# Kernel optimization log

Hardware: AMD Instinct MI355X
Metric: run time of the kernel (lower is better)

Reference implementation:

```python
import jax, jax.numpy as jnp
import numpy as np

N, F_IN, H, D = 4096, 512, 4, 64  # nodes, in_features, num_heads, head_dim (out_features = H*D = 256)
NEG_BIG = -9e15


def setup_inputs() -> dict:
    key = jax.random.key(0)
    k_x, k_adj, k_W, k_a = jax.random.split(key, 4)
    x = jax.random.normal(k_x, (N, F_IN), dtype=jnp.float32)
    adj = jax.random.randint(k_adj, (N, N), 0, 2, dtype=jnp.int32)
    # xavier_uniform-like scales
    W = jax.random.normal(k_W, (H, F_IN, D), dtype=jnp.float32) * np.float32((6.0 / (F_IN + D)) ** 0.5)
    a = jax.random.normal(k_a, (H, 2 * D), dtype=jnp.float32) * np.float32(0.1)
    bias = jnp.zeros((H * D,), dtype=jnp.float32)
    return {"x": x, "adj": adj, "W": W, "a": a, "bias": bias}


def reference(x, adj, W, a, bias):
    # Wx per head: [H, N, D]
    Wx = jnp.einsum('nf,hfd->hnd', x, W)
    # e[h,i,j] = leaky_relu(a[h,:D].Wx[h,i] + a[h,D:].Wx[h,j]) -- same math as concat form
    s_src = jnp.einsum('hnd,hd->hn', Wx, a[:, :D])  # [H, N]
    s_dst = jnp.einsum('hnd,hd->hn', Wx, a[:, D:])  # [H, N]
    e = jax.nn.leaky_relu(s_src[:, :, None] + s_dst[:, None, :], negative_slope=0.2)  # [H, N, N]
    masked = jnp.where(adj[None, :, :] > 0, e, jnp.float32(NEG_BIG))
    att = jax.nn.softmax(masked, axis=-1)  # row-wise softmax, [H, N, N]
    h = jnp.einsum('hij,hjd->hid', att, Wx)  # [H, N, D]
    out = h.transpose(1, 0, 2).reshape(x.shape[0], -1) + bias  # [N, H*D]
    return jax.nn.relu(out)
```

## Files before the change

### kernel.cpp

```cpp
#include <hip/hip_runtime.h>
#include <hip/hip_bf16.h>

#define NN   4096
#define FIN  512
#define NH   4
#define DD   64

typedef float f32x4 __attribute__((ext_vector_type(4)));
typedef short s16x8 __attribute__((ext_vector_type(8)));

__device__ __forceinline__ short bfbits(float f) {
  union { float f; unsigned u; } v; v.f = f;
  unsigned r = v.u + 0x7FFFu + ((v.u >> 16) & 1u);
  return (short)(r >> 16);
}

__device__ __forceinline__ int pkbf(float a, float b) {
  union { float f; unsigned u; } va, vb;
  va.f = a; vb.f = b;
  unsigned ra = (va.u + 0x7FFFu + ((va.u >> 16) & 1u)) >> 16;
  unsigned rb = (vb.u + 0x7FFFu + ((vb.u >> 16) & 1u)) & 0xFFFF0000u;
  return (int)(ra | rb);
}

__device__ __forceinline__ float hexp2(float x) {
#if __has_builtin(__builtin_amdgcn_exp2f)
  return __builtin_amdgcn_exp2f(x);
#else
  return __builtin_exp2f(x);
#endif
}

__global__ __launch_bounds__(512, 4) void gat_pre(
    const int* __restrict__ adj, const float* __restrict__ x,
    const float* __restrict__ W, const float* __restrict__ a,
    unsigned long long* __restrict__ bits, short* __restrict__ V2,
    float* __restrict__ ssrc, float* __restrict__ sdst)
{
  __shared__ __align__(16) char sm[34816];
  short* As = (short*)sm;
  short* Bs = (short*)(sm + 17408);
  float* Cs = (float*)sm;

  const int b = blockIdx.x;
  const int t = threadIdx.x;
  const int w = t >> 6, lane = t & 63;

  const int g3 = b / 3, m3 = b - g3 * 3;
  if (m3 < 2) {
    const int row = g3 * 2 + m3 + ((w) << 9);
    const int pb = g3 * 2 + m3;
    const int rrow = (pb << 3) | w;
    const int* arow = adj + (size_t)rrow * NN;
    unsigned long long mine = 0;
#pragma unroll 8
    for (int it = 0; it < 64; ++it) {
      int v = arow[it * 64 + lane];
      unsigned long long bl = __ballot(v != 0);
      if (lane == it) mine = bl;
    }
    bits[(size_t)rrow * 64 + lane] = mine;
    (void)row;
    return;
  }

  const int b2 = g3;
  const int h  = b2 >> 6;
  const int r  = b2 & 63;
  const int n0 = r * 64;
  const int lm = lane & 15, q = lane >> 4;
  const int rs = w & 3, cs = w >> 2;

  f32x4 acc[2] = {};
  const float* Wh = W + (size_t)h * (FIN * DD);

  for (int kq = 0; kq < 4; ++kq) {
    {
      const int row = t >> 3, fl = (t & 7) * 16;
      const float* xp = x + (size_t)(n0 + row) * FIN + kq * 128 + fl;
      float4 v0 = ((const float4*)xp)[0];
      float4 v1 = ((const float4*)xp)[1];
      float4 v2 = ((const float4*)xp)[2];
      float4 v3 = ((const float4*)xp)[3];
      union { short s[8]; int4 v; } u0, u1;
      u0.s[0]=bfbits(v0.x); u0.s[1]=bfbits(v0.y); u0.s[2]=bfbits(v0.z); u0.s[3]=bfbits(v0.w);
      u0.s[4]=bfbits(v1.x); u0.s[5]=bfbits(v1.y); u0.s[6]=bfbits(v1.z); u0.s[7]=bfbits(v1.w);
      u1.s[0]=bfbits(v2.x); u1.s[1]=bfbits(v2.y); u1.s[2]=bfbits(v2.z); u1.s[3]=bfbits(v2.w);
      u1.s[4]=bfbits(v3.x); u1.s[5]=bfbits(v3.y); u1.s[6]=bfbits(v3.z); u1.s[7]=bfbits(v3.w);
      *(int4*)(As + row * 136 + fl)     = u0.v;
      *(int4*)(As + row * 136 + fl + 8) = u1.v;
    }
    {
      const int fl = t >> 2, dc = (t & 3) * 16;
      const float* wp = Wh + (size_t)(kq * 128 + fl) * DD + dc;
      float4 w0 = ((const float4*)wp)[0];
      float4 w1 = ((const float4*)wp)[1];
      float4 w2 = ((const float4*)wp)[2];
      float4 w3 = ((const float4*)wp)[3];
      Bs[(dc+ 0)*136+fl]=bfbits(w0.x); Bs[(dc+ 1)*136+fl]=bfbits(w0.y);
      Bs[(dc+ 2)*136+fl]=bfbits(w0.z); Bs[(dc+ 3)*136+fl]=bfbits(w0.w);
      Bs[(dc+ 4)*136+fl]=bfbits(w1.x); Bs[(dc+ 5)*136+fl]=bfbits(w1.y);
      Bs[(dc+ 6)*136+fl]=bfbits(w1.z); Bs[(dc+ 7)*136+fl]=bfbits(w1.w);
      Bs[(dc+ 8)*136+fl]=bfbits(w2.x); Bs[(dc+ 9)*136+fl]=bfbits(w2.y);
      Bs[(dc+10)*136+fl]=bfbits(w2.z); Bs[(dc+11)*136+fl]=bfbits(w2.w);
      Bs[(dc+12)*136+fl]=bfbits(w3.x); Bs[(dc+13)*136+fl]=bfbits(w3.y);
      Bs[(dc+14)*136+fl]=bfbits(w3.z); Bs[(dc+15)*136+fl]=bfbits(w3.w);
    }
    __syncthreads();
#pragma unroll
    for (int s = 0; s < 4; ++s) {
      s16x8 af = *(const s16x8*)(As + (rs * 16 + lm) * 136 + s * 32 + q * 8);
#pragma unroll
      for (int c = 0; c < 2; ++c) {
        s16x8 bf = *(const s16x8*)(Bs + (cs * 32 + c * 16 + lm) * 136 + s * 32 + q * 8);
        acc[c] = __builtin_amdgcn_mfma_f32_16x16x32_bf16(af, bf, acc[c], 0, 0, 0);
      }
    }
    __syncthreads();
  }

#pragma unroll
  for (int c = 0; c < 2; ++c)
#pragma unroll
    for (int g = 0; g < 4; ++g)
      Cs[(cs * 32 + c * 16 + lm) * 65 + (rs * 16 + q * 4 + g)] = acc[c][g];
  __syncthreads();

  {
    const int d = t >> 3, nc = (t & 7) * 8;
    union { short s[8]; int4 v; } u;
#pragma unroll
    for (int e = 0; e < 8; ++e) u.s[e] = bfbits(Cs[d * 65 + nc + e]);
    *(int4*)(V2 + ((size_t)(h * 128 + r * 2 + (nc >> 5)) * 64 + d) * 32 + (nc & 31)) = u.v;
  }
  if (t < 128) {
    const int n = t & 63;
    const int isdst = t >> 6;
    const float* av = a + h * 128 + isdst * 64;
    float s = 0.f;
#pragma unroll 8
    for (int d = 0; d < 64; ++d) s = fmaf(Cs[d * 65 + n], av[d], s);
    const float LOG2E = 1.4426950408889634f;
    (isdst ? sdst : ssrc)[h * NN + n0 + n] = s * LOG2E;
  }
}

__global__ __launch_bounds__(512, 4) void gat_k2(
    const unsigned* __restrict__ bits, const short* __restrict__ V2,
    const float* __restrict__ ssrc, const float* __restrict__ sdst,
    const float* __restrict__ bias, float* __restrict__ out)
{
  __shared__ float MRG[4][32][68];
  __shared__ float Lm[8][32];

  const int b  = blockIdx.x;
  const int rt = b >> 2;
  const int h  = b & 3;
  const int t  = threadIdx.x;
  const int w  = t >> 6, lane = t & 63;
  const int lm = lane & 15, q = lane >> 4;
  const int jc = w;
  const int ib = rt * 32;
  const int i0 = ib + lm, i1 = i0 + 16;

  const float src0 = ssrc[h * NN + i0] - 1000.0f;
  const float src1 = ssrc[h * NN + i1] - 1000.0f;

  const short one = 0x3F80;
  s16x8 bones = {};
  if (lm == 0) {
    bones[0]=one; bones[1]=one; bones[2]=one; bones[3]=one;
    bones[4]=one; bones[5]=one; bones[6]=one; bones[7]=one;
  }

  f32x4 acc[2][4] = {};
  f32x4 accl[2] = {};

  const short*  Vb  = V2 + (size_t)h * 262144 + (size_t)jc * 16 * 2048
                      + lm * 32 + q * 8;
  const float*  sdh = sdst + h * NN + jc * 512 + q * 8;
  const unsigned* b0 = bits + (size_t)i0 * 128 + jc * 16;
  const unsigned* b1 = bits + (size_t)i1 * 128 + jc * 16;

  unsigned Wd0[4], Wd1[4], nWd0[4], nWd1[4];
  *(uint4*)Wd0 = ((const uint4*)b0)[0];
  *(uint4*)Wd1 = ((const uint4*)b1)[0];

  s16x8 bfc[4];
#pragma unroll
  for (int c = 0; c < 4; ++c) bfc[c] = *(const s16x8*)(Vb + c * 512);
  float4 S0 = ((const float4*)sdh)[0];
  float4 S1 = ((const float4*)(sdh + 4))[0];

  const int shq = q * 8;

  for (int s = 0; s < 4; ++s) {
    if (s < 3) {
      *(uint4*)nWd0 = ((const uint4*)b0)[s + 1];
      *(uint4*)nWd1 = ((const uint4*)b1)[s + 1];
    }
#pragma unroll
    for (int jsub = 0; jsub < 4; ++jsub) {
      const int js = s * 4 + jsub;
      const int jn = (js < 15) ? js + 1 : js;

      s16x8 bfn[4];
#pragma unroll
      for (int c = 0; c < 4; ++c)
        bfn[c] = *(const s16x8*)(Vb + jn * 2048 + c * 512);
      float4 T0 = ((const float4*)(sdh + jn * 32))[0];
      float4 T1 = ((const float4*)(sdh + jn * 32 + 4))[0];

      const unsigned wq0 = Wd0[jsub] >> shq;
      const unsigned wq1 = Wd1[jsub] >> shq;

#pragma unroll
      for (int rf = 0; rf < 2; ++rf) {
        const float src_i = rf ? src1 : src0;
        const unsigned wq = rf ? wq1 : wq0;
        float p[8];
#define PGEN(dv, e)                                                           \
        { float tp = src_i + (dv);                                            \
          float u  = fmaxf(tp, fmaf(tp, 0.2f, -800.0f));                      \
          u = fmaf((float)((wq >> (e)) & 1u), 1000.0f, u);                    \
          p[e] = hexp2(u); }
        PGEN(S0.x, 0) PGEN(S0.y, 1) PGEN(S0.z, 2) PGEN(S0.w, 3)
        PGEN(S1.x, 4) PGEN(S1.y, 5) PGEN(S1.z, 6) PGEN(S1.w, 7)
#undef PGEN
        union { int i4[4]; s16x8 v; } af;
        af.i4[0] = pkbf(p[0], p[1]);
        af.i4[1] = pkbf(p[2], p[3]);
        af.i4[2] = pkbf(p[4], p[5]);
        af.i4[3] = pkbf(p[6], p[7]);
#pragma unroll
        for (int c = 0; c < 4; ++c)
          acc[rf][c] = __builtin_amdgcn_mfma_f32_16x16x32_bf16(af.v, bfc[c], acc[rf][c], 0, 0, 0);
        accl[rf] = __builtin_amdgcn_mfma_f32_16x16x32_bf16(af.v, bones, accl[rf], 0, 0, 0);
      }
#pragma unroll
      for (int c = 0; c < 4; ++c) bfc[c] = bfn[c];
      S0 = T0; S1 = T1;
    }
#pragma unroll
    for (int e = 0; e < 4; ++e) { Wd0[e] = nWd0[e]; Wd1[e] = nWd1[e]; }
  }

  if (lm == 0) {
#pragma unroll
    for (int rf = 0; rf < 2; ++rf)
#pragma unroll
      for (int g = 0; g < 4; ++g)
        Lm[w][rf * 16 + q * 4 + g] = accl[rf][g];
  }
  if (w >= 4) {
#pragma unroll
    for (int rf = 0; rf < 2; ++rf)
#pragma unroll
      for (int c = 0; c < 4; ++c)
#pragma unroll
        for (int g = 0; g < 4; ++g)
          MRG[w - 4][rf * 16 + q * 4 + g][c * 16 + lm] = acc[rf][c][g];
  }
  __syncthreads();
  if (w < 4) {
#pragma unroll
    for (int rf = 0; rf < 2; ++rf)
#pragma unroll
      for (int c = 0; c < 4; ++c)
#pragma unroll
        for (int g = 0; g < 4; ++g)
          acc[rf][c][g] += MRG[w][rf * 16 + q * 4 + g][c * 16 + lm];
  }
  __syncthreads();
  if (w >= 1 && w < 4) {
#pragma unroll
    for (int rf = 0; rf < 2; ++rf)
#pragma unroll
      for (int c = 0; c < 4; ++c)
#pragma unroll
        for (int g = 0; g < 4; ++g)
          MRG[w - 1][rf * 16 + q * 4 + g][c * 16 + lm] = acc[rf][c][g];
  }
  __syncthreads();
  if (w == 0) {
#pragma unroll
    for (int rf = 0; rf < 2; ++rf) {
#pragma unroll
      for (int g = 0; g < 4; ++g) {
        const int row = rf * 16 + q * 4 + g;
        float l = 0.f;
#pragma unroll
        for (int ww = 0; ww < 8; ++ww) l += Lm[ww][row];
        const float inv = 1.0f / l;
        const int grow = ib + row;
#pragma unroll
        for (int c = 0; c < 4; ++c) {
          const int col = c * 16 + lm;
          float v = acc[rf][c][g]
                  + MRG[0][row][col] + MRG[1][row][col] + MRG[2][row][col];
          float o = fmaf(v, inv, bias[h * 64 + col]);
          out[(size_t)grow * 256 + h * 64 + col] = fmaxf(o, 0.0f);
        }
      }
    }
  }
}

extern "C" void kernel_launch(void* const* d_in, const int* in_sizes, int n_in,
                              void* d_out, int out_size, void* d_ws, size_t ws_size,
                              hipStream_t stream) {
  const float* x    = (const float*)d_in[0];
  const int*   adj  = (const int*)d_in[1];
  const float* W    = (const float*)d_in[2];
  const float* a    = (const float*)d_in[3];
  const float* bias = (const float*)d_in[4];
  float* out = (float*)d_out;

  short* V2 = (short*)d_ws;
  unsigned long long* bits =
      (unsigned long long*)((char*)d_ws + (size_t)2 * 1024 * 1024);
  float* ssrc = (float*)((char*)d_ws + (size_t)4 * 1024 * 1024);
  float* sdst = ssrc + NH * NN;

  gat_pre<<<768, 512, 0, stream>>>(adj, x, W, a, bits, V2, ssrc, sdst);
  gat_k2<<<512, 512, 0, stream>>>((const unsigned*)bits, V2, ssrc, sdst, bias, out);
}
```

Before: 137.9 us.

## Split attention kernel over two key halves and add a reduction kernel

The attention kernel now splits the key (j) range into two halves, so each block covers half the columns. This doubles the grid from 512 to 1024 blocks and shortens each block's loop. Partial numerators and row sums go to workspace, and a new finalize kernel adds the two halves, normalizes, applies bias and ReLU. The aim is more parallelism and better occupancy across the CUs, at the cost of an extra launch and about 8MB of partial-result traffic to and from global memory.

```diff
diff --git a/kernel.cpp b/kernel.cpp
--- a/kernel.cpp
+++ b/kernel.cpp
@@ -48,7 +48,6 @@
 
   const int g3 = b / 3, m3 = b - g3 * 3;
   if (m3 < 2) {
-    const int row = g3 * 2 + m3 + ((w) << 9);
     const int pb = g3 * 2 + m3;
     const int rrow = (pb << 3) | w;
     const int* arow = adj + (size_t)rrow * NN;
@@ -60,7 +59,6 @@
       if (lane == it) mine = bl;
     }
     bits[(size_t)rrow * 64 + lane] = mine;
-    (void)row;
     return;
   }
 
@@ -145,17 +143,18 @@
   }
 }
 
-__global__ __launch_bounds__(512, 4) void gat_k2(
+__global__ __launch_bounds__(512, 4) void gat_k2p(
     const unsigned* __restrict__ bits, const short* __restrict__ V2,
     const float* __restrict__ ssrc, const float* __restrict__ sdst,
-    const float* __restrict__ bias, float* __restrict__ out)
+    float* __restrict__ Pn, float* __restrict__ Pl)
 {
   __shared__ float MRG[4][32][68];
   __shared__ float Lm[8][32];
 
   const int b  = blockIdx.x;
-  const int rt = b >> 2;
-  const int h  = b & 3;
+  const int rt = b >> 3;
+  const int h  = (b >> 1) & 3;
+  const int jh = b & 1;
   const int t  = threadIdx.x;
   const int w  = t >> 6, lane = t & 63;
   const int lm = lane & 15, q = lane >> 4;
@@ -176,11 +175,12 @@
   f32x4 acc[2][4] = {};
   f32x4 accl[2] = {};
 
-  const short*  Vb  = V2 + (size_t)h * 262144 + (size_t)jc * 16 * 2048
+  const int jt0 = jh * 64 + jc * 8;
+  const short*  Vb  = V2 + (size_t)h * 262144 + (size_t)jt0 * 2048
                       + lm * 32 + q * 8;
-  const float*  sdh = sdst + h * NN + jc * 512 + q * 8;
-  const unsigned* b0 = bits + (size_t)i0 * 128 + jc * 16;
-  const unsigned* b1 = bits + (size_t)i1 * 128 + jc * 16;
+  const float*  sdh = sdst + h * NN + jt0 * 32 + q * 8;
+  const unsigned* b0 = bits + (size_t)i0 * 128 + jt0;
+  const unsigned* b1 = bits + (size_t)i1 * 128 + jt0;
 
   unsigned Wd0[4], Wd1[4], nWd0[4], nWd1[4];
   *(uint4*)Wd0 = ((const uint4*)b0)[0];
@@ -194,15 +194,15 @@
 
   const int shq = q * 8;
 
-  for (int s = 0; s < 4; ++s) {
-    if (s < 3) {
-      *(uint4*)nWd0 = ((const uint4*)b0)[s + 1];
-      *(uint4*)nWd1 = ((const uint4*)b1)[s + 1];
+  for (int s = 0; s < 2; ++s) {
+    if (s < 1) {
+      *(uint4*)nWd0 = ((const uint4*)b0)[1];
+      *(uint4*)nWd1 = ((const uint4*)b1)[1];
     }
 #pragma unroll
     for (int jsub = 0; jsub < 4; ++jsub) {
       const int js = s * 4 + jsub;
-      const int jn = (js < 15) ? js + 1 : js;
+      const int jn = (js < 7) ? js + 1 : js;
 
       s16x8 bfn[4];
 #pragma unroll
@@ -288,22 +288,48 @@
 #pragma unroll
       for (int g = 0; g < 4; ++g) {
         const int row = rf * 16 + q * 4 + g;
-        float l = 0.f;
-#pragma unroll
-        for (int ww = 0; ww < 8; ++ww) l += Lm[ww][row];
-        const float inv = 1.0f / l;
-        const int grow = ib + row;
+        if (lm == 0) {
+          float l = 0.f;
+#pragma unroll
+          for (int ww = 0; ww < 8; ++ww) l += Lm[ww][row];
+          Pl[(size_t)b * 32 + row] = l;
+        }
 #pragma unroll
         for (int c = 0; c < 4; ++c) {
           const int col = c * 16 + lm;
           float v = acc[rf][c][g]
                   + MRG[0][row][col] + MRG[1][row][col] + MRG[2][row][col];
-          float o = fmaf(v, inv, bias[h * 64 + col]);
-          out[(size_t)grow * 256 + h * 64 + col] = fmaxf(o, 0.0f);
+          Pn[((size_t)b * 32 + row) * 64 + col] = v;
         }
       }
     }
   }
+}
+
+__global__ __launch_bounds__(256) void gat_fin(
+    const float* __restrict__ Pn, const float* __restrict__ Pl,
+    const float* __restrict__ bias, float* __restrict__ out)
+{
+  const int f = blockIdx.x * 256 + threadIdx.x;
+  const int row = f >> 6;
+  const int c4  = f & 63;
+  const int h   = c4 >> 4;
+  const int cd  = (c4 & 15) * 4;
+  const int rt  = row >> 5, r32 = row & 31;
+
+  const int pb0 = ((rt * 4 + h) << 1);
+  const size_t base0 = ((size_t)pb0 * 32 + r32) * 64 + cd;
+  float4 n0 = *(const float4*)(Pn + base0);
+  float4 n1 = *(const float4*)(Pn + base0 + 32 * 64);
+  const float l = Pl[(size_t)pb0 * 32 + r32] + Pl[(size_t)(pb0 + 1) * 32 + r32];
+  const float inv = 1.0f / l;
+  float4 bv = *(const float4*)(bias + h * 64 + cd);
+  float4 o;
+  o.x = fmaxf(fmaf(n0.x + n1.x, inv, bv.x), 0.f);
+  o.y = fmaxf(fmaf(n0.y + n1.y, inv, bv.y), 0.f);
+  o.z = fmaxf(fmaf(n0.z + n1.z, inv, bv.z), 0.f);
+  o.w = fmaxf(fmaf(n0.w + n1.w, inv, bv.w), 0.f);
+  *(float4*)(out + (size_t)row * 256 + h * 64 + cd) = o;
 }
 
 extern "C" void kernel_launch(void* const* d_in, const int* in_sizes, int n_in,
@@ -321,7 +347,10 @@
       (unsigned long long*)((char*)d_ws + (size_t)2 * 1024 * 1024);
   float* ssrc = (float*)((char*)d_ws + (size_t)4 * 1024 * 1024);
   float* sdst = ssrc + NH * NN;
+  float* Pn   = (float*)((char*)d_ws + (size_t)5 * 1024 * 1024);
+  float* Pl   = (float*)((char*)d_ws + (size_t)13 * 1024 * 1024);
 
   gat_pre<<<768, 512, 0, stream>>>(adj, x, W, a, bits, V2, ssrc, sdst);
-  gat_k2<<<512, 512, 0, stream>>>((const unsigned*)bits, V2, ssrc, sdst, bias, out);
-}
+  gat_k2p<<<1024, 512, 0, stream>>>((const unsigned*)bits, V2, ssrc, sdst, Pn, Pl);
+  gat_fin<<<1024, 256, 0, stream>>>(Pn, Pl, bias, out);
+}
```

After: 143.1 us. +3.8%, slower.
